# Performance work log

Measured on AMD Instinct MI355X. Metric: run time of the kernel, lower is better.

## Reference

```python
import jax, jax.numpy as jnp
import numpy as np

D = 11           # num_classes + 1 (embedding dim)
HL = 7           # window height = 1 + 2*H_PAD
WL = 7           # window width  = 1 + 2*W_PAD
PAD = 3
MAXH, MAXW = 30, 30
FF = 64          # dim_feedforward
EPS = 1e-5       # LayerNorm eps (torch default)
PAD_VALUE = 0.0


def setup_inputs() -> dict:
    key = jax.random.key(0)
    ks = jax.random.split(key, 6)
    N, C, H, W = 1, 10, 16, 16
    s = 0.1
    return {
        "x": jax.random.uniform(ks[0], (N, C, H, W), jnp.float32),
        "Wqkv": jax.random.normal(ks[1], (3 * D, D), jnp.float32) * s,  # in_proj_weight
        "Wo": jax.random.normal(ks[2], (D, D), jnp.float32) * s,        # out_proj.weight
        "W1": jax.random.normal(ks[3], (FF, D), jnp.float32) * s,       # linear1.weight
        "W2": jax.random.normal(ks[4], (D, FF), jnp.float32) * s,       # linear2.weight
        "ln1_w": jnp.ones((D,), jnp.float32),                           # norm1.weight (bias=False)
        "ln2_w": jnp.ones((D,), jnp.float32),                           # norm2.weight (bias=False)
    }


def _layer_norm(x, w):
    m = jnp.mean(x, axis=-1, keepdims=True)
    v = jnp.mean(jnp.square(x - m), axis=-1, keepdims=True)
    return (x - m) / jnp.sqrt(v + EPS) * w


def _encoder_layer(x, Wqkv, Wo, W1, W2, ln1_w, ln2_w):
    # x: [B, S, D]; post-norm, 1 head, no biases, eval mode (dropout off)
    qkv = x @ Wqkv.T
    q, k, v = jnp.split(qkv, 3, axis=-1)
    scale = 1.0 / jnp.sqrt(jnp.float32(D))
    attn = jax.nn.softmax(jnp.einsum('bqd,bkd->bqk', q, k) * scale, axis=-1)
    sa = jnp.einsum('bqk,bkd->bqd', attn, v) @ Wo.T
    x = _layer_norm(x + sa, ln1_w)
    ff = jax.nn.relu(x @ W1.T) @ W2.T
    return _layer_norm(x + ff, ln2_w)


def reference(x, Wqkv, Wo, W1, W2, ln1_w, ln2_w):
    N, C, H, W = x.shape
    C1 = C + 1
    # mask channel: 1 in the padded border, 0 inside
    mask = jnp.pad(jnp.zeros((N, 1, H, W), x.dtype),
                   ((0, 0), (0, 0), (PAD, PAD), (PAD, PAD)), constant_values=1.0)
    xp = jnp.pad(x, ((0, 0), (0, 0), (PAD, PAD), (PAD, PAD)), constant_values=PAD_VALUE)
    xp = jnp.concatenate([xp, mask], axis=1)            # [N, C+1, H+6, W+6]
    win = jnp.stack([xp[:, :, i:i + H, j:j + W]
                     for i in range(HL) for j in range(WL)], axis=-1)  # [N, C1, H, W, 49]
    win = jnp.transpose(win, (0, 2, 3, 1, 4))           # [N, H, W, C1, 49]
    win = win.reshape(N * H * W * C1, HL, WL)
    # embed window into max_height x max_width canvas (rest = pad_value)
    canvas = jnp.full((N * H * W * C1, MAXH, MAXW), PAD_VALUE, x.dtype)
    canvas = canvas.at[:, :HL, :WL].set(win)
    seq = canvas.reshape(N * H * W, C1, MAXH * MAXW).transpose(0, 2, 1)  # [B, S=900, D=11]
    out = _encoder_layer(seq, Wqkv, Wo, W1, W2, ln1_w, ln2_w)
    return out.transpose(0, 2, 1)[:, :-1]               # [B, C, 900]
```

## Files before the change

### kernel.cpp

```cpp
#include <hip/hip_runtime.h>


#define D 11
#define ROWP 12
#define NW 49
#define NR 50
#define NWP 52
#define FFD 64
#define W2P 68
#define HP  68
#define CIN 10
#define SEQ 900
#define NB 256
#define TPB 832

__device__ __forceinline__ float dot12(const float4* a, const float4* b) {
    float4 s = make_float4(0.f, 0.f, 0.f, 0.f);
    #pragma unroll
    for (int i = 0; i < 3; ++i) {
        float4 x = a[i], y = b[i];
        s.x += x.x * y.x; s.y += x.y * y.y; s.z += x.z * y.z; s.w += x.w * y.w;
    }
    return s.x + s.y + s.z + s.w;
}

__device__ __forceinline__ void wave_sync() {
    __builtin_amdgcn_wave_barrier();
    asm volatile("s_waitcnt lgkmcnt(0)" ::: "memory");
    __builtin_amdgcn_wave_barrier();
}

__global__ __launch_bounds__(TPB) void pve_kernel(
    const float* __restrict__ gx,
    const float* __restrict__ gWqkv,
    const float* __restrict__ gWo,
    const float* __restrict__ gW1,
    const float* __restrict__ gW2,
    const float* __restrict__ gln1,
    const float* __restrict__ gln2,
    float* __restrict__ out)
{
    __shared__ __align__(16) float sQ[33 * ROWP];
    __shared__ __align__(16) float sWo[D * ROWP];
    __shared__ __align__(16) float sW1[FFD * ROWP];
    __shared__ __align__(16) float sW2[D * W2P];
    __shared__ __align__(16) float sSeq[NR][ROWP];
    __shared__ __align__(16) float sK[NW][ROWP];
    __shared__ __align__(16) float sVt[D][NWP];
    __shared__ __align__(16) float sQr[NR][ROWP];
    __shared__ __align__(16) float sE[NR][NWP];
    __shared__ __align__(16) float sNum[NR][ROWP];
    __shared__ __align__(16) float sX1n[NR][ROWP];
    __shared__ __align__(16) float sH[NR][HP];
    __shared__ __align__(16) float sR[NR][ROWP];

    const int tid = threadIdx.x;
    const int b = blockIdx.x;
    const int h = b >> 4;
    const int w = b & 15;

    const int r = tid >> 4;
    const int d = tid & 15;
    const bool rowv = (r < NR);
    const bool dv = (d < D);

    for (int i = tid; i < 33 * ROWP; i += TPB) {
        const int rr = i / ROWP, cc = i - rr * ROWP;
        sQ[i] = (cc < D) ? gWqkv[rr * D + cc] : 0.f;
    }
    for (int i = tid; i < D * ROWP; i += TPB) {
        const int rr = i / ROWP, cc = i - rr * ROWP;
        sWo[i] = (cc < D) ? gWo[rr * D + cc] : 0.f;
    }
    for (int i = tid; i < FFD * ROWP; i += TPB) {
        const int rr = i / ROWP, cc = i - rr * ROWP;
        sW1[i] = (cc < D) ? gW1[rr * D + cc] : 0.f;
    }
    for (int i = tid; i < D * W2P; i += TPB) {
        const int rr = i / W2P, cc = i - rr * W2P;
        sW2[i] = (cc < FFD) ? gW2[rr * FFD + cc] : 0.f;
    }
    float lnw1 = 0.f, lnw2 = 0.f;
    if (dv) { lnw1 = gln1[d]; lnw2 = gln2[d]; }

    float xin = 0.f;
    if (rowv) {
        if (dv) {
            if (r < NW) {
                const int i7 = r / 7, j7 = r - i7 * 7;
                const int y = h + i7, xx = w + j7;
                const bool inter = (y >= 3) && (y < 19) && (xx >= 3) && (xx < 19);
                const int base = inter ? ((y - 3) * 16 + (xx - 3)) : 0;
                if (d < CIN) xin = inter ? gx[d * 256 + base] : 0.0f;
                else         xin = inter ? 0.0f : 1.0f;
            }
            sSeq[r][d] = xin;
        } else if (d == D) {
            sSeq[r][D] = 0.f;
        }
    }
    __syncthreads();

    if (rowv) {
        if (dv) {
            const float4* sv = (const float4*)&sSeq[r][0];
            const float aq = dot12(sv, (const float4*)&sQ[d * ROWP]);
            const float ak = dot12(sv, (const float4*)&sQ[(D + d) * ROWP]);
            const float av = dot12(sv, (const float4*)&sQ[(2 * D + d) * ROWP]);
            sQr[r][d] = aq;
            if (r < NW) { sK[r][d] = ak; sVt[d][r] = av; }
            else { sVt[d][NW] = 0.f; sVt[d][NW + 1] = 0.f; sVt[d][NW + 2] = 0.f; }
        } else if (d == D) {
            sQr[r][D] = 0.f;
            if (r < NW) sK[r][D] = 0.f;
        }
    }
    __syncthreads();

    float den = 851.0f;
    if (rowv) {
        const float scale = 0.30151134457776363f;
        const float4* qv = (const float4*)&sQr[r][0];
        const float4 q0 = qv[0], q1 = qv[1], q2 = qv[2];
        float psum = 0.f;
        #pragma unroll
        for (int it = 0; it < 4; ++it) {
            const int tt = d + (it << 4);
            if (tt < NWP) {
                float e = 0.f;
                if (tt < NW) {
                    const float4* kv = (const float4*)&sK[tt][0];
                    const float4 k0 = kv[0], k1 = kv[1], k2 = kv[2];
                    const float s =
                        q0.x*k0.x + q0.y*k0.y + q0.z*k0.z + q0.w*k0.w +
                        q1.x*k1.x + q1.y*k1.y + q1.z*k1.z + q1.w*k1.w +
                        q2.x*k2.x + q2.y*k2.y + q2.z*k2.z + q2.w*k2.w;
                    e = __expf(s * scale);
                }
                sE[r][tt] = e;
                psum += e;
            }
        }
        psum += __shfl_xor(psum, 8, 16);
        psum += __shfl_xor(psum, 4, 16);
        psum += __shfl_xor(psum, 2, 16);
        psum += __shfl_xor(psum, 1, 16);
        den += psum;
    }
    wave_sync();

    if (rowv) {
        if (dv) {
            const float4* ev = (const float4*)&sE[r][0];
            const float4* vv = (const float4*)&sVt[d][0];
            float4 an = make_float4(0.f, 0.f, 0.f, 0.f);
            #pragma unroll
            for (int i = 0; i < 13; ++i) {
                const float4 e = ev[i], v = vv[i];
                an.x += e.x * v.x; an.y += e.y * v.y;
                an.z += e.z * v.z; an.w += e.w * v.w;
            }
            sNum[r][d] = an.x + an.y + an.z + an.w;
        } else if (d == D) {
            sNum[r][D] = 0.f;
        }
    }
    wave_sync();

    float x1 = 0.f;
    if (rowv && dv) {
        const float acc = dot12((const float4*)&sNum[r][0],
                                (const float4*)&sWo[d * ROWP]);
        x1 = xin + acc / den;
    }
    {
        float s1 = x1, s2 = x1 * x1;
        s1 += __shfl_xor(s1, 8, 16); s2 += __shfl_xor(s2, 8, 16);
        s1 += __shfl_xor(s1, 4, 16); s2 += __shfl_xor(s2, 4, 16);
        s1 += __shfl_xor(s1, 2, 16); s2 += __shfl_xor(s2, 2, 16);
        s1 += __shfl_xor(s1, 1, 16); s2 += __shfl_xor(s2, 1, 16);
        const float m   = s1 * (1.0f / 11.0f);
        const float var = s2 * (1.0f / 11.0f) - m * m;
        x1 = (x1 - m) * rsqrtf(var + 1e-5f) * lnw1;
    }
    if (rowv) {
        if (dv) sX1n[r][d] = x1;
        else if (d == D) sX1n[r][D] = 0.f;
    }
    wave_sync();

    if (rowv) {
        const float4* xv = (const float4*)&sX1n[r][0];
        const float4 xa = xv[0], xb = xv[1], xc = xv[2];
        #pragma unroll
        for (int it = 0; it < 4; ++it) {
            const int ff = d + (it << 4);
            const float4* wv = (const float4*)&sW1[ff * ROWP];
            const float4 w0 = wv[0], w1 = wv[1], w2 = wv[2];
            const float acc =
                xa.x*w0.x + xa.y*w0.y + xa.z*w0.z + xa.w*w0.w +
                xb.x*w1.x + xb.y*w1.y + xb.z*w1.z + xb.w*w1.w +
                xc.x*w2.x + xc.y*w2.y + xc.z*w2.z + xc.w*w2.w;
            sH[r][ff] = fmaxf(acc, 0.0f);
        }
    }
    wave_sync();

    float yv = 0.f;
    if (rowv && dv) {
        const float4* hv = (const float4*)&sH[r][0];
        const float4* wv = (const float4*)&sW2[d * W2P];
        float4 a4 = make_float4(0.f, 0.f, 0.f, 0.f);
        #pragma unroll
        for (int i = 0; i < 16; ++i) {
            const float4 hh = hv[i], ww = wv[i];
            a4.x += hh.x * ww.x; a4.y += hh.y * ww.y;
            a4.z += hh.z * ww.z; a4.w += hh.w * ww.w;
        }
        yv = x1 + a4.x + a4.y + a4.z + a4.w;
    }
    {
        float s1 = yv, s2 = yv * yv;
        s1 += __shfl_xor(s1, 8, 16); s2 += __shfl_xor(s2, 8, 16);
        s1 += __shfl_xor(s1, 4, 16); s2 += __shfl_xor(s2, 4, 16);
        s1 += __shfl_xor(s1, 2, 16); s2 += __shfl_xor(s2, 2, 16);
        s1 += __shfl_xor(s1, 1, 16); s2 += __shfl_xor(s2, 1, 16);
        const float m   = s1 * (1.0f / 11.0f);
        const float var = s2 * (1.0f / 11.0f) - m * m;
        if (rowv && dv) sR[r][d] = (yv - m) * rsqrtf(var + 1e-5f) * lnw2;
    }
    __syncthreads();

    float4* ob4 = (float4*)(out + b * (CIN * SEQ));
    #pragma unroll
    for (int k = 0; k < 3; ++k) {
        const int qi = tid + k * TPB;
        if (qi < 2250) {
            const int c  = qi / 225;
            const int s0 = (qi - c * 225) * 4;
            float4 v4;
            float* pv = (float*)&v4;
            #pragma unroll
            for (int u = 0; u < 4; ++u) {
                const int s = s0 + u;
                const int i = s / 30;
                const int j = s - i * 30;
                pv[u] = (i < 7 && j < 7) ? sR[i * 7 + j][c] : sR[NW][c];
            }
            ob4[qi] = v4;
        }
    }
}

extern "C" void kernel_launch(void* const* d_in, const int* in_sizes, int n_in,
                              void* d_out, int out_size, void* d_ws, size_t ws_size,
                              hipStream_t stream) {
    (void)in_sizes; (void)n_in; (void)out_size; (void)d_ws; (void)ws_size;
    const float* x    = (const float*)d_in[0];
    const float* Wqkv = (const float*)d_in[1];
    const float* Wo   = (const float*)d_in[2];
    const float* W1   = (const float*)d_in[3];
    const float* W2   = (const float*)d_in[4];
    const float* ln1  = (const float*)d_in[5];
    const float* ln2  = (const float*)d_in[6];
    pve_kernel<<<NB, TPB, 0, stream>>>(x, Wqkv, Wo, W1, W2, ln1, ln2,
                                       (float*)d_out);
}
```

Before: 75.00 us.

## Replace per-row shared-memory staging with register shuffles and transposed W2

```diff
diff --git a/kernel.cpp b/kernel.cpp
--- a/kernel.cpp
+++ b/kernel.cpp
@@ -5,30 +5,25 @@
 #define ROWP 12
 #define NW 49
 #define NR 50
-#define NWP 52
 #define FFD 64
-#define W2P 68
-#define HP  68
 #define CIN 10
 #define SEQ 900
 #define NB 256
 #define TPB 832
 
-__device__ __forceinline__ float dot12(const float4* a, const float4* b) {
-    float4 s = make_float4(0.f, 0.f, 0.f, 0.f);
-    #pragma unroll
-    for (int i = 0; i < 3; ++i) {
-        float4 x = a[i], y = b[i];
-        s.x += x.x * y.x; s.y += x.y * y.y; s.z += x.z * y.z; s.w += x.w * y.w;
-    }
-    return s.x + s.y + s.z + s.w;
-}
-
-__device__ __forceinline__ void wave_sync() {
-    __builtin_amdgcn_wave_barrier();
-    asm volatile("s_waitcnt lgkmcnt(0)" ::: "memory");
-    __builtin_amdgcn_wave_barrier();
-}
+#define FMA11(P, E, A0, A1, A2) \
+    P[0] += (E)*(A0).x; P[1] += (E)*(A0).y; P[2] += (E)*(A0).z; P[3] += (E)*(A0).w; \
+    P[4] += (E)*(A1).x; P[5] += (E)*(A1).y; P[6] += (E)*(A1).z; P[7] += (E)*(A1).w; \
+    P[8] += (E)*(A2).x; P[9] += (E)*(A2).y; P[10] += (E)*(A2).z;
+
+#define DOT11(Q, A0, A1, A2) \
+    ((Q)[0]*(A0).x + (Q)[1]*(A0).y + (Q)[2]*(A0).z + (Q)[3]*(A0).w + \
+     (Q)[4]*(A1).x + (Q)[5]*(A1).y + (Q)[6]*(A1).z + (Q)[7]*(A1).w + \
+     (Q)[8]*(A2).x + (Q)[9]*(A2).y + (Q)[10]*(A2).z)
+
+#define RED16(X) \
+    X += __shfl_xor(X, 8, 16); X += __shfl_xor(X, 4, 16); \
+    X += __shfl_xor(X, 2, 16); X += __shfl_xor(X, 1, 16);
 
 __global__ __launch_bounds__(TPB) void pve_kernel(
     const float* __restrict__ gx,
@@ -43,15 +38,9 @@
     __shared__ __align__(16) float sQ[33 * ROWP];
     __shared__ __align__(16) float sWo[D * ROWP];
     __shared__ __align__(16) float sW1[FFD * ROWP];
-    __shared__ __align__(16) float sW2[D * W2P];
-    __shared__ __align__(16) float sSeq[NR][ROWP];
+    __shared__ __align__(16) float sW2t[FFD * ROWP];
     __shared__ __align__(16) float sK[NW][ROWP];
-    __shared__ __align__(16) float sVt[D][NWP];
-    __shared__ __align__(16) float sQr[NR][ROWP];
-    __shared__ __align__(16) float sE[NR][NWP];
-    __shared__ __align__(16) float sNum[NR][ROWP];
-    __shared__ __align__(16) float sX1n[NR][ROWP];
-    __shared__ __align__(16) float sH[NR][HP];
+    __shared__ __align__(16) float sV[NW][ROWP];
     __shared__ __align__(16) float sR[NR][ROWP];
 
     const int tid = threadIdx.x;
@@ -68,6 +57,38 @@
         const int rr = i / ROWP, cc = i - rr * ROWP;
         sQ[i] = (cc < D) ? gWqkv[rr * D + cc] : 0.f;
     }
+    float lnw1 = 0.f, lnw2 = 0.f;
+    if (dv) { lnw1 = gln1[d]; lnw2 = gln2[d]; }
+
+    float xin = 0.f;
+    if (rowv && dv && r < NW) {
+        const int i7 = r / 7, j7 = r - i7 * 7;
+        const int y = h + i7, xx = w + j7;
+        const bool inter = (y >= 3) && (y < 19) && (xx >= 3) && (xx < 19);
+        const int base = inter ? ((y - 3) * 16 + (xx - 3)) : 0;
+        if (d < CIN) xin = inter ? gx[d * 256 + base] : 0.0f;
+        else         xin = inter ? 0.0f : 1.0f;
+    }
+    __syncthreads();
+
+    float aq = 0.f;
+    if (rowv) {
+        float sx[11];
+        #pragma unroll
+        for (int dd = 0; dd < 11; ++dd) sx[dd] = __shfl(xin, dd, 16);
+        if (dv) {
+            const float4* qa = (const float4*)&sQ[d * ROWP];
+            const float4* ka = (const float4*)&sQ[(D + d) * ROWP];
+            const float4* va = (const float4*)&sQ[(2 * D + d) * ROWP];
+            const float4 q0 = qa[0], q1 = qa[1], q2 = qa[2];
+            const float4 k0 = ka[0], k1 = ka[1], k2 = ka[2];
+            const float4 v0 = va[0], v1 = va[1], v2 = va[2];
+            aq = DOT11(sx, q0, q1, q2);
+            const float ak = DOT11(sx, k0, k1, k2);
+            const float av = DOT11(sx, v0, v1, v2);
+            if (r < NW) { sK[r][d] = ak; sV[r][d] = av; }
+        }
+    }
     for (int i = tid; i < D * ROWP; i += TPB) {
         const int rr = i / ROWP, cc = i - rr * ROWP;
         sWo[i] = (cc < D) ? gWo[rr * D + cc] : 0.f;
@@ -76,158 +97,103 @@
         const int rr = i / ROWP, cc = i - rr * ROWP;
         sW1[i] = (cc < D) ? gW1[rr * D + cc] : 0.f;
     }
-    for (int i = tid; i < D * W2P; i += TPB) {
-        const int rr = i / W2P, cc = i - rr * W2P;
-        sW2[i] = (cc < FFD) ? gW2[rr * FFD + cc] : 0.f;
-    }
-    float lnw1 = 0.f, lnw2 = 0.f;
-    if (dv) { lnw1 = gln1[d]; lnw2 = gln2[d]; }
-
-    float xin = 0.f;
-    if (rowv) {
-        if (dv) {
-            if (r < NW) {
-                const int i7 = r / 7, j7 = r - i7 * 7;
-                const int y = h + i7, xx = w + j7;
-                const bool inter = (y >= 3) && (y < 19) && (xx >= 3) && (xx < 19);
-                const int base = inter ? ((y - 3) * 16 + (xx - 3)) : 0;
-                if (d < CIN) xin = inter ? gx[d * 256 + base] : 0.0f;
-                else         xin = inter ? 0.0f : 1.0f;
+    for (int i = tid; i < FFD * ROWP; i += TPB) {
+        const int ff = i / ROWP, cc = i - ff * ROWP;
+        sW2t[i] = (cc < D) ? gW2[cc * FFD + ff] : 0.f;
+    }
+    __syncthreads();
+
+    float den = 851.0f;
+    float ev[4] = {0.f, 0.f, 0.f, 0.f};
+    if (rowv) {
+        const float scale = 0.30151134457776363f;
+        float q[11];
+        #pragma unroll
+        for (int dd = 0; dd < 11; ++dd) q[dd] = __shfl(aq, dd, 16);
+        #pragma unroll
+        for (int it = 0; it < 4; ++it) {
+            const int tt = d + (it << 4);
+            if (tt < NW) {
+                const float4* kp = (const float4*)&sK[tt][0];
+                const float4 k0 = kp[0], k1 = kp[1], k2 = kp[2];
+                const float s = DOT11(q, k0, k1, k2);
+                ev[it] = __expf(s * scale);
             }
-            sSeq[r][d] = xin;
-        } else if (d == D) {
-            sSeq[r][D] = 0.f;
-        }
-    }
-    __syncthreads();
-
-    if (rowv) {
-        if (dv) {
-            const float4* sv = (const float4*)&sSeq[r][0];
-            const float aq = dot12(sv, (const float4*)&sQ[d * ROWP]);
-            const float ak = dot12(sv, (const float4*)&sQ[(D + d) * ROWP]);
-            const float av = dot12(sv, (const float4*)&sQ[(2 * D + d) * ROWP]);
-            sQr[r][d] = aq;
-            if (r < NW) { sK[r][d] = ak; sVt[d][r] = av; }
-            else { sVt[d][NW] = 0.f; sVt[d][NW + 1] = 0.f; sVt[d][NW + 2] = 0.f; }
-        } else if (d == D) {
-            sQr[r][D] = 0.f;
-            if (r < NW) sK[r][D] = 0.f;
-        }
-    }
-    __syncthreads();
-
-    float den = 851.0f;
-    if (rowv) {
-        const float scale = 0.30151134457776363f;
-        const float4* qv = (const float4*)&sQr[r][0];
-        const float4 q0 = qv[0], q1 = qv[1], q2 = qv[2];
-        float psum = 0.f;
+        }
+        float ps = ev[0] + ev[1] + ev[2] + ev[3];
+        RED16(ps);
+        den += ps;
+    }
+
+    float num[11] = {0.f,0.f,0.f,0.f,0.f,0.f,0.f,0.f,0.f,0.f,0.f};
+    if (rowv) {
         #pragma unroll
         for (int it = 0; it < 4; ++it) {
             const int tt = d + (it << 4);
-            if (tt < NWP) {
-                float e = 0.f;
-                if (tt < NW) {
-                    const float4* kv = (const float4*)&sK[tt][0];
-                    const float4 k0 = kv[0], k1 = kv[1], k2 = kv[2];
-                    const float s =
-                        q0.x*k0.x + q0.y*k0.y + q0.z*k0.z + q0.w*k0.w +
-                        q1.x*k1.x + q1.y*k1.y + q1.z*k1.z + q1.w*k1.w +
-                        q2.x*k2.x + q2.y*k2.y + q2.z*k2.z + q2.w*k2.w;
-                    e = __expf(s * scale);
-                }
-                sE[r][tt] = e;
-                psum += e;
+            if (tt < NW) {
+                const float4* vp = (const float4*)&sV[tt][0];
+                const float4 v0 = vp[0], v1 = vp[1], v2 = vp[2];
+                const float e = ev[it];
+                FMA11(num, e, v0, v1, v2);
             }
         }
-        psum += __shfl_xor(psum, 8, 16);
-        psum += __shfl_xor(psum, 4, 16);
-        psum += __shfl_xor(psum, 2, 16);
-        psum += __shfl_xor(psum, 1, 16);
-        den += psum;
-    }
-    wave_sync();
-
-    if (rowv) {
-        if (dv) {
-            const float4* ev = (const float4*)&sE[r][0];
-            const float4* vv = (const float4*)&sVt[d][0];
-            float4 an = make_float4(0.f, 0.f, 0.f, 0.f);
-            #pragma unroll
-            for (int i = 0; i < 13; ++i) {
-                const float4 e = ev[i], v = vv[i];
-                an.x += e.x * v.x; an.y += e.y * v.y;
-                an.z += e.z * v.z; an.w += e.w * v.w;
-            }
-            sNum[r][d] = an.x + an.y + an.z + an.w;
-        } else if (d == D) {
-            sNum[r][D] = 0.f;
-        }
-    }
-    wave_sync();
+        #pragma unroll
+        for (int dd = 0; dd < 11; ++dd) { RED16(num[dd]); }
+    }
 
     float x1 = 0.f;
     if (rowv && dv) {
-        const float acc = dot12((const float4*)&sNum[r][0],
-                                (const float4*)&sWo[d * ROWP]);
+        const float4* wp = (const float4*)&sWo[d * ROWP];
+        const float4 w0 = wp[0], w1 = wp[1], w2 = wp[2];
+        const float acc = DOT11(num, w0, w1, w2);
         x1 = xin + acc / den;
     }
     {
         float s1 = x1, s2 = x1 * x1;
-        s1 += __shfl_xor(s1, 8, 16); s2 += __shfl_xor(s2, 8, 16);
-        s1 += __shfl_xor(s1, 4, 16); s2 += __shfl_xor(s2, 4, 16);
-        s1 += __shfl_xor(s1, 2, 16); s2 += __shfl_xor(s2, 2, 16);
-        s1 += __shfl_xor(s1, 1, 16); s2 += __shfl_xor(s2, 1, 16);
+        RED16(s1); RED16(s2);
         const float m   = s1 * (1.0f / 11.0f);
         const float var = s2 * (1.0f / 11.0f) - m * m;
         x1 = (x1 - m) * rsqrtf(var + 1e-5f) * lnw1;
     }
-    if (rowv) {
-        if (dv) sX1n[r][d] = x1;
-        else if (d == D) sX1n[r][D] = 0.f;
-    }
-    wave_sync();
-
-    if (rowv) {
-        const float4* xv = (const float4*)&sX1n[r][0];
-        const float4 xa = xv[0], xb = xv[1], xc = xv[2];
+
+    float hh[4] = {0.f, 0.f, 0.f, 0.f};
+    if (rowv) {
+        float xb[11];
+        #pragma unroll
+        for (int dd = 0; dd < 11; ++dd) xb[dd] = __shfl(x1, dd, 16);
         #pragma unroll
         for (int it = 0; it < 4; ++it) {
             const int ff = d + (it << 4);
-            const float4* wv = (const float4*)&sW1[ff * ROWP];
-            const float4 w0 = wv[0], w1 = wv[1], w2 = wv[2];
-            const float acc =
-                xa.x*w0.x + xa.y*w0.y + xa.z*w0.z + xa.w*w0.w +
-                xb.x*w1.x + xb.y*w1.y + xb.z*w1.z + xb.w*w1.w +
-                xc.x*w2.x + xc.y*w2.y + xc.z*w2.z + xc.w*w2.w;
-            sH[r][ff] = fmaxf(acc, 0.0f);
-        }
-    }
-    wave_sync();
-
-    float yv = 0.f;
-    if (rowv && dv) {
-        const float4* hv = (const float4*)&sH[r][0];
-        const float4* wv = (const float4*)&sW2[d * W2P];
-        float4 a4 = make_float4(0.f, 0.f, 0.f, 0.f);
-        #pragma unroll
-        for (int i = 0; i < 16; ++i) {
-            const float4 hh = hv[i], ww = wv[i];
-            a4.x += hh.x * ww.x; a4.y += hh.y * ww.y;
-            a4.z += hh.z * ww.z; a4.w += hh.w * ww.w;
-        }
-        yv = x1 + a4.x + a4.y + a4.z + a4.w;
-    }
+            const float4* wp = (const float4*)&sW1[ff * ROWP];
+            const float4 w0 = wp[0], w1 = wp[1], w2 = wp[2];
+            hh[it] = fmaxf(DOT11(xb, w0, w1, w2), 0.0f);
+        }
+    }
+
+    float p2[11] = {0.f,0.f,0.f,0.f,0.f,0.f,0.f,0.f,0.f,0.f,0.f};
+    if (rowv) {
+        #pragma unroll
+        for (int it = 0; it < 4; ++it) {
+            const int f = d + (it << 4);
+            const float4* wp = (const float4*)&sW2t[f * ROWP];
+            const float4 w0 = wp[0], w1 = wp[1], w2 = wp[2];
+            const float e = hh[it];
+            FMA11(p2, e, w0, w1, w2);
+        }
+        #pragma unroll
+        for (int dd = 0; dd < 11; ++dd) { RED16(p2[dd]); }
+    }
+    float ysel = 0.f;
+    #pragma unroll
+    for (int dd = 0; dd < 11; ++dd) ysel = (d == dd) ? p2[dd] : ysel;
+    const float y = x1 + ysel;
+
     {
-        float s1 = yv, s2 = yv * yv;
-        s1 += __shfl_xor(s1, 8, 16); s2 += __shfl_xor(s2, 8, 16);
-        s1 += __shfl_xor(s1, 4, 16); s2 += __shfl_xor(s2, 4, 16);
-        s1 += __shfl_xor(s1, 2, 16); s2 += __shfl_xor(s2, 2, 16);
-        s1 += __shfl_xor(s1, 1, 16); s2 += __shfl_xor(s2, 1, 16);
+        float s1 = y, s2 = y * y;
+        RED16(s1); RED16(s2);
         const float m   = s1 * (1.0f / 11.0f);
         const float var = s2 * (1.0f / 11.0f) - m * m;
-        if (rowv && dv) sR[r][d] = (yv - m) * rsqrtf(var + 1e-5f) * lnw2;
+        if (rowv && dv) sR[r][d] = (y - m) * rsqrtf(var + 1e-5f) * lnw2;
     }
     __syncthreads();
 
```

Result: slower. 79.22 us (+5.6%).
